# Kernel tuning notes

Measured on AMD Instinct MI355X. Metric: run time of the kernel, lower is better.

Reference implementation:

```python
import jax, jax.numpy as jnp
import numpy as np


def conv1x1(x, w, b):
    # 1x1 Conv2d: x [B,C,H,W], w [O,C], b [O] -> [B,O,H,W]
    return jnp.einsum('bchw,oc->bohw', x, w) + b[None, :, None, None]


def setup_inputs() -> dict:
    key = jax.random.key(0)
    ks = jax.random.split(key, 10)
    B, C, Ci, H, W = 4, 64, 32, 64, 64
    s = 0.05
    return {
        'supp_feature': jax.random.normal(ks[0], (B, C, H, W), jnp.float32),
        'ref_feature': jax.random.normal(ks[1], (B, C, H, W), jnp.float32),
        'theta_w': jax.random.normal(ks[2], (Ci, C), jnp.float32) * s,
        'theta_b': jax.random.normal(ks[3], (Ci,), jnp.float32) * s,
        'phi_w': jax.random.normal(ks[4], (Ci, C), jnp.float32) * s,
        'phi_b': jax.random.normal(ks[5], (Ci,), jnp.float32) * s,
        'g_w': jax.random.normal(ks[6], (Ci, C), jnp.float32) * s,
        'g_b': jax.random.normal(ks[7], (Ci,), jnp.float32) * s,
        'w_w': jax.random.normal(ks[8], (C, Ci), jnp.float32) * s,
        'w_b': jax.random.normal(ks[9], (C,), jnp.float32) * s,
    }


def reference(supp_feature, ref_feature, theta_w, theta_b, phi_w, phi_b,
              g_w, g_b, w_w, w_b):
    B, C, H, W = supp_feature.shape
    Ci = theta_w.shape[0]
    N = H * W
    theta_x = conv1x1(supp_feature, theta_w, theta_b).reshape(B, Ci, N)  # [B,Ci,N]
    phi_y = conv1x1(ref_feature, phi_w, phi_b).reshape(B, Ci, N)        # [B,Ci,M]
    g_y = conv1x1(ref_feature, g_w, g_b).reshape(B, Ci, N)              # [B,Ci,M]
    # f[b,n,m] = <theta_x[b,:,n], phi_y[b,:,m]>  (unscaled)
    f = jnp.einsum('bcn,bcm->bnm', theta_x, phi_y)
    # NOTE: softmax over dim=1 (the QUERY axis n), matching F.softmax(f, dim=1)
    f_div_C = jax.nn.softmax(f, axis=1)
    # x1[b,c,n] = sum_m f_div_C[b,n,m] * g_y[b,c,m]
    x1 = jnp.einsum('bnm,bcm->bcn', f_div_C, g_y).reshape(B, Ci, H, W)
    z = supp_feature + conv1x1(x1, w_w, w_b)
    return z
```

## Files before the change

kernel.cpp:

```cpp
#include <hip/hip_runtime.h>

#define C_ 64
#define CI_ 32
#define N_ 4096
#define LOG2E 1.4426950408889634f

typedef __attribute__((ext_vector_type(8))) short bf16x8;
typedef __attribute__((ext_vector_type(4))) float f32x4;

__device__ __forceinline__ unsigned short f2bf_rne(float f) {
  unsigned u = __builtin_bit_cast(unsigned, f);
  unsigned r = (u + 0x7FFFu + ((u >> 16) & 1u)) >> 16;
  return (unsigned short)r;
}
__device__ __forceinline__ unsigned pack_bf2(float lo, float hi) {
  unsigned a = (__builtin_bit_cast(unsigned, lo) + 0x8000u) >> 16;
  unsigned b = (__builtin_bit_cast(unsigned, hi) + 0x8000u) & 0xFFFF0000u;
  return a | b;
}
__device__ __forceinline__ void dma16(const void* gp, const void* lp) {
  __builtin_amdgcn_global_load_lds(
      (const __attribute__((address_space(1))) unsigned*)(unsigned long long)gp,
      (__attribute__((address_space(3))) unsigned*)(unsigned)(unsigned long long)lp,
      16, 0, 0);
}


__global__ __launch_bounds__(256) void k1_proj(
    const float* __restrict__ supp, const float* __restrict__ ref,
    const float* __restrict__ tw, const float* __restrict__ tb,
    const float* __restrict__ pw, const float* __restrict__ pb,
    const float* __restrict__ gw, const float* __restrict__ gb,
    unsigned short* __restrict__ theta, unsigned short* __restrict__ phi2,
    unsigned short* __restrict__ g2, float* __restrict__ den)
{
  const int proj = blockIdx.x >> 8;
  const int rr = blockIdx.x & 255;
  const int b = rr >> 6;
  const int n0 = (rr & 63) << 6;
  const int o = __builtin_amdgcn_readfirstlane(threadIdx.x >> 6);
  const int lane = threadIdx.x & 63;
  const int n = n0 + lane;

  if (blockIdx.x < 16) {
    uint4 z = {0u, 0u, 0u, 0u};
    *(uint4*)(den + blockIdx.x * 1024 + threadIdx.x * 4) = z;
  }

  __shared__ float gL[CI_][66];

  const float *W, *bias, *src;
  if (proj == 0)      { W = tw; bias = tb; src = supp; }
  else if (proj == 1) { W = pw; bias = pb; src = ref; }
  else                { W = gw; bias = gb; src = ref; }

  const float* x = src + (size_t)b * (C_ * N_) + n;
  const float* Wo = W + o * 8 * C_;
  float acc[8];
#pragma unroll
  for (int k = 0; k < 8; k++) acc[k] = bias[o * 8 + k];
#pragma unroll 8
  for (int c = 0; c < C_; c++) {
    float v = x[(size_t)c * N_];
#pragma unroll
    for (int k = 0; k < 8; k++) acc[k] = fmaf(Wo[k * C_ + c], v, acc[k]);
  }

  if (proj == 0) {
    unsigned pk[4];
#pragma unroll
    for (int k = 0; k < 4; k++)
      pk[k] = (unsigned)f2bf_rne(acc[2 * k] * LOG2E) |
              ((unsigned)f2bf_rne(acc[2 * k + 1] * LOG2E) << 16);
    *(uint4*)(theta + (((size_t)b * N_ + n) << 5) + o * 8) = *(uint4*)pk;
  } else if (proj == 1) {
    unsigned pk[4];
#pragma unroll
    for (int k = 0; k < 4; k++)
      pk[k] = (unsigned)f2bf_rne(acc[2 * k]) |
              ((unsigned)f2bf_rne(acc[2 * k + 1]) << 16);
    size_t off = (((size_t)b * 128 + (n >> 5)) << 10) + o * 256 + (n & 31) * 8;
    *(uint4*)(phi2 + off) = *(uint4*)pk;
  } else {
#pragma unroll
    for (int k = 0; k < 8; k++) gL[o * 8 + k][lane] = acc[k];
    __syncthreads();
    const int t = threadIdx.x;
    const int c = t >> 7;
    const int rr2 = t & 127;
    const int q = rr2 >> 5;
    const int i = rr2 & 31;
    const float* g0 = &gL[i][c * 32 + 4 * q];
    unsigned pk[4];
    pk[0] = pack_bf2(g0[0], g0[1]);
    pk[1] = pack_bf2(g0[2], g0[3]);
    pk[2] = pack_bf2(g0[16], g0[17]);
    pk[3] = pack_bf2(g0[18], g0[19]);
    size_t off = (((size_t)b * 128 + (n0 >> 5) + c) << 10) + rr2 * 8;
    *(uint4*)(g2 + off) = *(uint4*)pk;
  }
}

__global__ __launch_bounds__(256) void k2_den(
    const unsigned short* __restrict__ theta, const unsigned short* __restrict__ phi2,
    const float* __restrict__ ww, float* __restrict__ den,
    unsigned short* __restrict__ ww2)
{
  const int mt = blockIdx.x & 63;
  const int nq = (blockIdx.x >> 6) & 3;
  const int b = blockIdx.x >> 8;
  const int tid = threadIdx.x;
  const int w = tid >> 6;
  const int lane = tid & 63;
  const int row16 = lane & 15;
  const int quad = lane >> 4;

  if (blockIdx.x == 0) {
    for (int e = tid; e < C_ * CI_; e += 256) {
      int p = e & 31;
      int i = 4 * ((p >> 3) & 3) + (p & 3) + 16 * ((p >> 2) & 1);
      ww2[e] = f2bf_rne(ww[(e >> 5) * CI_ + i]);
    }
  }

  __shared__ __align__(16) unsigned short TH[2][2048];

  bf16x8 bf = *(const bf16x8*)(phi2 +
      (((size_t)b * 128 + mt * 2 + (w >> 1)) << 10) + (quad << 8) +
      ((w & 1) * 16 + row16) * 8);

  const unsigned short* thbase = theta + (((size_t)b * N_ + nq * 1024) << 5);

  dma16(thbase + w * 512 + lane * 8, &TH[0][w * 512]);
  __syncthreads();

  f32x4 zero = {0.f, 0.f, 0.f, 0.f};
  float ds4[4] = {0.f, 0.f, 0.f, 0.f};

  for (int ph = 0; ph < 16; ph++) {
    const int buf = ph & 1;
    if (ph + 1 < 16)
      dma16(thbase + (ph + 1) * 2048 + w * 512 + lane * 8, &TH[buf ^ 1][w * 512]);
#pragma unroll
    for (int s = 0; s < 4; s++) {
      bf16x8 af = *(const bf16x8*)(&TH[buf][s * 512 + row16 * 32 + quad * 8]);
      f32x4 ff = __builtin_amdgcn_mfma_f32_16x16x32_bf16(af, bf, zero, 0, 0, 0);
#pragma unroll
      for (int r = 0; r < 4; r++) ds4[r] += __builtin_amdgcn_exp2f(ff[r]);
    }
    __syncthreads();
  }

  float v = (ds4[0] + ds4[1]) + (ds4[2] + ds4[3]);
  v += __shfl_xor(v, 16);
  v += __shfl_xor(v, 32);
  if (lane < 16) {
    int ml64 = w * 16 + lane;
    int ch = mt * 2 + (ml64 >> 5);
    int local = ml64 & 31;
    int q = (local & 15) >> 2;
    int j = (local & 3) | (((local >> 4) & 1) << 2);
    atomicAdd(&den[(((size_t)b * 128 + ch) << 5) + 8 * q + j], v);
  }
}

__global__ __launch_bounds__(1024) void k3_attn(
    const unsigned short* __restrict__ theta, const unsigned short* __restrict__ phi2,
    const unsigned short* __restrict__ g2, const float* __restrict__ den,
    const unsigned short* __restrict__ ww2, const float* __restrict__ wb,
    const float* __restrict__ supp, float* __restrict__ out)
{
  const int tid = threadIdx.x;
  const int w = tid >> 6;
  const int lane = tid & 63;
  const int p = blockIdx.x;
  const int b = (p & 7) >> 1;
  const int t = ((p >> 3) << 1) | (p & 1);
  const int n0 = t << 6;
  const int ns = w & 3;
  const int q = w >> 2;
  const int row16 = lane & 15;
  const int quad = lane >> 4;

  __shared__ __align__(16) unsigned short SB[2][4][4096];
  __shared__ float ldL[4096];

  for (int e = tid; e < 4096; e += 1024)
    ldL[e] = -__log2f(den[((size_t)b << 12) + e]);

  bf16x8 tB = *(const bf16x8*)(theta +
      (((size_t)b * N_ + n0 + ns * 16 + row16) << 5) + (quad << 3));

  const size_t chb = (size_t)b * 128;
  const int sq = w >> 2;

  f32x4 zero = {0.f, 0.f, 0.f, 0.f};
  f32x4 xa = zero, xb = zero;

#pragma unroll
  for (int s = 0; s < 2; s++) {
    int idx = w * 2 + s;
    int cc = (idx >> 2) & 1;
    int part = idx & 3;
    const unsigned short* src = (part >= 2 ? g2 : phi2) +
        ((chb + sq * 32 + cc) << 10) + ((size_t)(part & 1) << 9) + lane * 8;
    dma16(src, &SB[0][sq][cc * 2048 + (part >= 2 ? 1024 : 0) + ((part & 1) << 9)]);
  }
  __syncthreads();

  for (int ph = 0; ph < 16; ph++) {
    const int buf = ph & 1;
    if (ph + 1 < 16) {
#pragma unroll
      for (int s = 0; s < 2; s++) {
        int idx = w * 2 + s;
        int cc = (idx >> 2) & 1;
        int part = idx & 3;
        const unsigned short* src = (part >= 2 ? g2 : phi2) +
            ((chb + sq * 32 + (ph + 1) * 2 + cc) << 10) + ((size_t)(part & 1) << 9) + lane * 8;
        dma16(src, &SB[buf ^ 1][sq][cc * 2048 + (part >= 2 ? 1024 : 0) + ((part & 1) << 9)]);
      }
    }
#pragma unroll
    for (int cc = 0; cc < 2; cc++) {
      const unsigned short* base = &SB[buf][q][cc * 2048];
      bf16x8 pA0 = *(const bf16x8*)(base + (quad << 8) + row16 * 8);
      bf16x8 pA1 = *(const bf16x8*)(base + (quad << 8) + (row16 + 16) * 8);
      bf16x8 gA0 = *(const bf16x8*)(base + 1024 + (quad << 8) + row16 * 8);
      bf16x8 gA1 = *(const bf16x8*)(base + 1024 + (quad << 8) + (row16 + 16) * 8);
      const float* lp = &ldL[((q * 32 + ph * 2 + cc) << 5) + (quad << 3)];
      f32x4 l0 = *(const f32x4*)lp;
      f32x4 l1 = *(const f32x4*)(lp + 4);

      f32x4 f0 = __builtin_amdgcn_mfma_f32_16x16x32_bf16(pA0, tB, l0, 0, 0, 0);
      f32x4 f1 = __builtin_amdgcn_mfma_f32_16x16x32_bf16(pA1, tB, l1, 0, 0, 0);

      uint4 d;
      d.x = pack_bf2(__builtin_amdgcn_exp2f(f0[0]), __builtin_amdgcn_exp2f(f0[1]));
      d.y = pack_bf2(__builtin_amdgcn_exp2f(f0[2]), __builtin_amdgcn_exp2f(f0[3]));
      d.z = pack_bf2(__builtin_amdgcn_exp2f(f1[0]), __builtin_amdgcn_exp2f(f1[1]));
      d.w = pack_bf2(__builtin_amdgcn_exp2f(f1[2]), __builtin_amdgcn_exp2f(f1[3]));
      bf16x8 Pb = __builtin_bit_cast(bf16x8, d);

      xa = __builtin_amdgcn_mfma_f32_16x16x32_bf16(gA0, Pb, xa, 0, 0, 0);
      xb = __builtin_amdgcn_mfma_f32_16x16x32_bf16(gA1, Pb, xb, 0, 0, 0);
    }
    __syncthreads();
  }

  float* part = (float*)SB;
  if (q) {
    float* dst = part + ((((q - 1) * 4 + ns) * 64 + lane) << 3);
#pragma unroll
    for (int r = 0; r < 4; r++) { dst[r] = xa[r]; dst[4 + r] = xb[r]; }
  }
  __syncthreads();
  if (q == 0) {
#pragma unroll
    for (int e = 0; e < 3; e++) {
      const float* s = part + (((e * 4 + ns) * 64 + lane) << 3);
#pragma unroll
      for (int r = 0; r < 4; r++) { xa[r] += s[r]; xb[r] += s[4 + r]; }
    }
    uint4 d;
    d.x = pack_bf2(xa[0], xa[1]);
    d.y = pack_bf2(xa[2], xa[3]);
    d.z = pack_bf2(xb[0], xb[1]);
    d.w = pack_bf2(xb[2], xb[3]);
    bf16x8 Bx = __builtin_bit_cast(bf16x8, d);
    const int nloc = n0 + ns * 16 + row16;
#pragma unroll
    for (int ct = 0; ct < 4; ct++) {
      bf16x8 aw = *(const bf16x8*)(ww2 + (ct * 16 + row16) * CI_ + (quad << 3));
      f32x4 o = __builtin_amdgcn_mfma_f32_16x16x32_bf16(aw, Bx, zero, 0, 0, 0);
#pragma unroll
      for (int r = 0; r < 4; r++) {
        int c = ct * 16 + quad * 4 + r;
        size_t ob = ((size_t)b * C_ + c) * N_ + nloc;
        out[ob] = o[r] + wb[c] + supp[ob];
      }
    }
  }
}

extern "C" void kernel_launch(void* const* d_in, const int* in_sizes, int n_in,
                              void* d_out, int out_size, void* d_ws, size_t ws_size,
                              hipStream_t stream)
{
  const float* supp = (const float*)d_in[0];
  const float* ref  = (const float*)d_in[1];
  const float* tw   = (const float*)d_in[2];
  const float* tb   = (const float*)d_in[3];
  const float* pw   = (const float*)d_in[4];
  const float* pb   = (const float*)d_in[5];
  const float* gw   = (const float*)d_in[6];
  const float* gb   = (const float*)d_in[7];
  const float* ww   = (const float*)d_in[8];
  const float* wb   = (const float*)d_in[9];
  float* out = (float*)d_out;

  char* ws = (char*)d_ws;
  unsigned short* theta = (unsigned short*)ws;
  unsigned short* phi2  = (unsigned short*)(ws + (1u << 20));
  unsigned short* g2    = (unsigned short*)(ws + (2u << 20));
  float*          den   = (float*)(ws + (3u << 20));
  unsigned short* ww2   = (unsigned short*)(ws + (3u << 20) + 65536);

  hipLaunchKernelGGL(k1_proj, dim3(768), dim3(256), 0, stream,
                     supp, ref, tw, tb, pw, pb, gw, gb, theta, phi2, g2, den);
  hipLaunchKernelGGL(k2_den, dim3(1024), dim3(256), 0, stream,
                     theta, phi2, ww, den, ww2);
  hipLaunchKernelGGL(k3_attn, dim3(256), dim3(1024), 0, stream,
                     theta, phi2, g2, den, ww2, wb, supp, out);
}
```

Measured before the change: 112.8 us.

## Fuse phi/g projections sharing ref loads and double pipeline stage depth

The projection kernel now computes phi and g in the same block, so each ref feature value is loaded once and feeds both weight sets. The grid shrinks from 768 to 512 blocks and the w_w bf16 conversion moves into it. The den and attention kernels double the size of each double-buffered stage, halving the number of loop iterations and barriers. This raises LDS use in k3 to 128KB for SB, which may cut occupancy or hit LDS limits.

```diff
diff --git a/kernel.cpp b/kernel.cpp
--- a/kernel.cpp
+++ b/kernel.cpp
@@ -31,10 +31,12 @@
     const float* __restrict__ tw, const float* __restrict__ tb,
     const float* __restrict__ pw, const float* __restrict__ pb,
     const float* __restrict__ gw, const float* __restrict__ gb,
+    const float* __restrict__ ww,
     unsigned short* __restrict__ theta, unsigned short* __restrict__ phi2,
-    unsigned short* __restrict__ g2, float* __restrict__ den)
+    unsigned short* __restrict__ g2, float* __restrict__ den,
+    unsigned short* __restrict__ ww2)
 {
-  const int proj = blockIdx.x >> 8;
+  const int pg = blockIdx.x >> 8;
   const int rr = blockIdx.x & 255;
   const int b = rr >> 6;
   const int n0 = (rr & 63) << 6;
@@ -46,44 +48,59 @@
     uint4 z = {0u, 0u, 0u, 0u};
     *(uint4*)(den + blockIdx.x * 1024 + threadIdx.x * 4) = z;
   }
+  if (blockIdx.x == 16) {
+    for (int e = threadIdx.x; e < C_ * CI_; e += 256) {
+      int p = e & 31;
+      int i = 4 * ((p >> 3) & 3) + (p & 3) + 16 * ((p >> 2) & 1);
+      ww2[e] = f2bf_rne(ww[(e >> 5) * CI_ + i]);
+    }
+  }
 
   __shared__ float gL[CI_][66];
 
-  const float *W, *bias, *src;
-  if (proj == 0)      { W = tw; bias = tb; src = supp; }
-  else if (proj == 1) { W = pw; bias = pb; src = ref; }
-  else                { W = gw; bias = gb; src = ref; }
-
-  const float* x = src + (size_t)b * (C_ * N_) + n;
-  const float* Wo = W + o * 8 * C_;
-  float acc[8];
-#pragma unroll
-  for (int k = 0; k < 8; k++) acc[k] = bias[o * 8 + k];
+  if (pg == 0) {
+    const float* x = supp + (size_t)b * (C_ * N_) + n;
+    const float* Wo = tw + o * 8 * C_;
+    float acc[8];
+#pragma unroll
+    for (int k = 0; k < 8; k++) acc[k] = tb[o * 8 + k];
 #pragma unroll 8
-  for (int c = 0; c < C_; c++) {
-    float v = x[(size_t)c * N_];
-#pragma unroll
-    for (int k = 0; k < 8; k++) acc[k] = fmaf(Wo[k * C_ + c], v, acc[k]);
-  }
-
-  if (proj == 0) {
+    for (int c = 0; c < C_; c++) {
+      float v = x[(size_t)c * N_];
+#pragma unroll
+      for (int k = 0; k < 8; k++) acc[k] = fmaf(Wo[k * C_ + c], v, acc[k]);
+    }
     unsigned pk[4];
 #pragma unroll
     for (int k = 0; k < 4; k++)
       pk[k] = (unsigned)f2bf_rne(acc[2 * k] * LOG2E) |
               ((unsigned)f2bf_rne(acc[2 * k + 1] * LOG2E) << 16);
     *(uint4*)(theta + (((size_t)b * N_ + n) << 5) + o * 8) = *(uint4*)pk;
-  } else if (proj == 1) {
+  } else {
+    const float* x = ref + (size_t)b * (C_ * N_) + n;
+    const float* Po = pw + o * 8 * C_;
+    const float* Go = gw + o * 8 * C_;
+    float ap[8], ag[8];
+#pragma unroll
+    for (int k = 0; k < 8; k++) { ap[k] = pb[o * 8 + k]; ag[k] = gb[o * 8 + k]; }
+#pragma unroll 8
+    for (int c = 0; c < C_; c++) {
+      float v = x[(size_t)c * N_];
+#pragma unroll
+      for (int k = 0; k < 8; k++) ap[k] = fmaf(Po[k * C_ + c], v, ap[k]);
+#pragma unroll
+      for (int k = 0; k < 8; k++) ag[k] = fmaf(Go[k * C_ + c], v, ag[k]);
+    }
     unsigned pk[4];
 #pragma unroll
     for (int k = 0; k < 4; k++)
-      pk[k] = (unsigned)f2bf_rne(acc[2 * k]) |
-              ((unsigned)f2bf_rne(acc[2 * k + 1]) << 16);
+      pk[k] = (unsigned)f2bf_rne(ap[2 * k]) |
+              ((unsigned)f2bf_rne(ap[2 * k + 1]) << 16);
     size_t off = (((size_t)b * 128 + (n >> 5)) << 10) + o * 256 + (n & 31) * 8;
     *(uint4*)(phi2 + off) = *(uint4*)pk;
-  } else {
-#pragma unroll
-    for (int k = 0; k < 8; k++) gL[o * 8 + k][lane] = acc[k];
+
+#pragma unroll
+    for (int k = 0; k < 8; k++) gL[o * 8 + k][lane] = ag[k];
     __syncthreads();
     const int t = threadIdx.x;
     const int c = t >> 7;
@@ -91,20 +108,19 @@
     const int q = rr2 >> 5;
     const int i = rr2 & 31;
     const float* g0 = &gL[i][c * 32 + 4 * q];
-    unsigned pk[4];
-    pk[0] = pack_bf2(g0[0], g0[1]);
-    pk[1] = pack_bf2(g0[2], g0[3]);
-    pk[2] = pack_bf2(g0[16], g0[17]);
-    pk[3] = pack_bf2(g0[18], g0[19]);
-    size_t off = (((size_t)b * 128 + (n0 >> 5) + c) << 10) + rr2 * 8;
-    *(uint4*)(g2 + off) = *(uint4*)pk;
+    unsigned gk[4];
+    gk[0] = pack_bf2(g0[0], g0[1]);
+    gk[1] = pack_bf2(g0[2], g0[3]);
+    gk[2] = pack_bf2(g0[16], g0[17]);
+    gk[3] = pack_bf2(g0[18], g0[19]);
+    size_t goff = (((size_t)b * 128 + (n0 >> 5) + c) << 10) + rr2 * 8;
+    *(uint4*)(g2 + goff) = *(uint4*)gk;
   }
 }
 
 __global__ __launch_bounds__(256) void k2_den(
     const unsigned short* __restrict__ theta, const unsigned short* __restrict__ phi2,
-    const float* __restrict__ ww, float* __restrict__ den,
-    unsigned short* __restrict__ ww2)
+    float* __restrict__ den)
 {
   const int mt = blockIdx.x & 63;
   const int nq = (blockIdx.x >> 6) & 3;
@@ -115,15 +131,7 @@
   const int row16 = lane & 15;
   const int quad = lane >> 4;
 
-  if (blockIdx.x == 0) {
-    for (int e = tid; e < C_ * CI_; e += 256) {
-      int p = e & 31;
-      int i = 4 * ((p >> 3) & 3) + (p & 3) + 16 * ((p >> 2) & 1);
-      ww2[e] = f2bf_rne(ww[(e >> 5) * CI_ + i]);
-    }
-  }
-
-  __shared__ __align__(16) unsigned short TH[2][2048];
+  __shared__ __align__(16) unsigned short TH[2][4096];
 
   bf16x8 bf = *(const bf16x8*)(phi2 +
       (((size_t)b * 128 + mt * 2 + (w >> 1)) << 10) + (quad << 8) +
@@ -131,18 +139,24 @@
 
   const unsigned short* thbase = theta + (((size_t)b * N_ + nq * 1024) << 5);
 
-  dma16(thbase + w * 512 + lane * 8, &TH[0][w * 512]);
+#pragma unroll
+  for (int s = 0; s < 2; s++)
+    dma16(thbase + (w * 2 + s) * 512 + lane * 8, &TH[0][(w * 2 + s) * 512]);
   __syncthreads();
 
   f32x4 zero = {0.f, 0.f, 0.f, 0.f};
   float ds4[4] = {0.f, 0.f, 0.f, 0.f};
 
-  for (int ph = 0; ph < 16; ph++) {
+  for (int ph = 0; ph < 8; ph++) {
     const int buf = ph & 1;
-    if (ph + 1 < 16)
-      dma16(thbase + (ph + 1) * 2048 + w * 512 + lane * 8, &TH[buf ^ 1][w * 512]);
-#pragma unroll
-    for (int s = 0; s < 4; s++) {
+    if (ph + 1 < 8) {
+#pragma unroll
+      for (int s = 0; s < 2; s++)
+        dma16(thbase + (ph + 1) * 4096 + (w * 2 + s) * 512 + lane * 8,
+              &TH[buf ^ 1][(w * 2 + s) * 512]);
+    }
+#pragma unroll
+    for (int s = 0; s < 8; s++) {
       bf16x8 af = *(const bf16x8*)(&TH[buf][s * 512 + row16 * 32 + quad * 8]);
       f32x4 ff = __builtin_amdgcn_mfma_f32_16x16x32_bf16(af, bf, zero, 0, 0, 0);
 #pragma unroll
@@ -182,7 +196,7 @@
   const int row16 = lane & 15;
   const int quad = lane >> 4;
 
-  __shared__ __align__(16) unsigned short SB[2][4][4096];
+  __shared__ __align__(16) unsigned short SB[2][4][8192];
   __shared__ float ldL[4096];
 
   for (int e = tid; e < 4096; e += 1024)
@@ -192,43 +206,37 @@
       (((size_t)b * N_ + n0 + ns * 16 + row16) << 5) + (quad << 3));
 
   const size_t chb = (size_t)b * 128;
-  const int sq = w >> 2;
 
   f32x4 zero = {0.f, 0.f, 0.f, 0.f};
   f32x4 xa = zero, xb = zero;
 
-#pragma unroll
-  for (int s = 0; s < 2; s++) {
-    int idx = w * 2 + s;
-    int cc = (idx >> 2) & 1;
-    int part = idx & 3;
-    const unsigned short* src = (part >= 2 ? g2 : phi2) +
-        ((chb + sq * 32 + cc) << 10) + ((size_t)(part & 1) << 9) + lane * 8;
-    dma16(src, &SB[0][sq][cc * 2048 + (part >= 2 ? 1024 : 0) + ((part & 1) << 9)]);
+
+#pragma unroll
+  for (int s = 0; s < 4; s++) {
+    const unsigned short* src = (s >= 2 ? g2 : phi2) +
+        ((chb + q * 32 + ns) << 10) + ((size_t)(s & 1) << 9) + lane * 8;
+    dma16(src, &SB[0][q][ns * 2048 + (s >= 2 ? 1024 : 0) + ((s & 1) << 9)]);
   }
   __syncthreads();
 
-  for (int ph = 0; ph < 16; ph++) {
+  for (int ph = 0; ph < 8; ph++) {
     const int buf = ph & 1;
-    if (ph + 1 < 16) {
-#pragma unroll
-      for (int s = 0; s < 2; s++) {
-        int idx = w * 2 + s;
-        int cc = (idx >> 2) & 1;
-        int part = idx & 3;
-        const unsigned short* src = (part >= 2 ? g2 : phi2) +
-            ((chb + sq * 32 + (ph + 1) * 2 + cc) << 10) + ((size_t)(part & 1) << 9) + lane * 8;
-        dma16(src, &SB[buf ^ 1][sq][cc * 2048 + (part >= 2 ? 1024 : 0) + ((part & 1) << 9)]);
+    if (ph + 1 < 8) {
+#pragma unroll
+      for (int s = 0; s < 4; s++) {
+        const unsigned short* src = (s >= 2 ? g2 : phi2) +
+            ((chb + q * 32 + (ph + 1) * 4 + ns) << 10) + ((size_t)(s & 1) << 9) + lane * 8;
+        dma16(src, &SB[buf ^ 1][q][ns * 2048 + (s >= 2 ? 1024 : 0) + ((s & 1) << 9)]);
       }
     }
 #pragma unroll
-    for (int cc = 0; cc < 2; cc++) {
+    for (int cc = 0; cc < 4; cc++) {
       const unsigned short* base = &SB[buf][q][cc * 2048];
       bf16x8 pA0 = *(const bf16x8*)(base + (quad << 8) + row16 * 8);
       bf16x8 pA1 = *(const bf16x8*)(base + (quad << 8) + (row16 + 16) * 8);
       bf16x8 gA0 = *(const bf16x8*)(base + 1024 + (quad << 8) + row16 * 8);
       bf16x8 gA1 = *(const bf16x8*)(base + 1024 + (quad << 8) + (row16 + 16) * 8);
-      const float* lp = &ldL[((q * 32 + ph * 2 + cc) << 5) + (quad << 3)];
+      const float* lp = &ldL[((q * 32 + ph * 4 + cc) << 5) + (quad << 3)];
       f32x4 l0 = *(const f32x4*)lp;
       f32x4 l1 = *(const f32x4*)(lp + 4);
 
@@ -306,10 +314,11 @@
   float*          den   = (float*)(ws + (3u << 20));
   unsigned short* ww2   = (unsigned short*)(ws + (3u << 20) + 65536);
 
-  hipLaunchKernelGGL(k1_proj, dim3(768), dim3(256), 0, stream,
-                     supp, ref, tw, tb, pw, pb, gw, gb, theta, phi2, g2, den);
+  hipLaunchKernelGGL(k1_proj, dim3(512), dim3(256), 0, stream,
+                     supp, ref, tw, tb, pw, pb, gw, gb, ww,
+                     theta, phi2, g2, den, ww2);
   hipLaunchKernelGGL(k2_den, dim3(1024), dim3(256), 0, stream,
-                     theta, phi2, ww, den, ww2);
+                     theta, phi2, den);
   hipLaunchKernelGGL(k3_attn, dim3(256), dim3(1024), 0, stream,
                      theta, phi2, g2, den, ww2, wb, supp, out);
 }
```

Result: slower. 116.7 us (+3.4%).
